# Performance work log

Hardware: AMD Instinct MI355X
Metric: run time of the kernel (lower is better)

The kernel has to match this reference:

```python
import jax, jax.numpy as jnp
import numpy as np

NUM_HEADS = 16

def alibi_slopes(num_heads):
    # 1 / ((2**8)**(1/H))**(i+1) for i in range(H)  -> shape (H, 1, 1)
    x = (2.0 ** 8) ** (1.0 / num_heads)
    return (1.0 / x ** (jnp.arange(1, num_heads + 1, dtype=jnp.float32)))[:, None, None]

def setup_inputs() -> dict:
    key = jax.random.key(0)
    k1, k2, k3 = jax.random.split(key, 3)
    B, T, D = 4, 2048, 1024
    x = jax.random.normal(k1, (B, T, D), dtype=jnp.float32)
    w_qkv = jax.random.normal(k2, (D, 3 * D), dtype=jnp.float32) * 0.02
    w_o = jax.random.normal(k3, (D, D), dtype=jnp.float32) * 0.02
    return {"x": x, "w_qkv": w_qkv, "w_o": w_o}

def reference(x, w_qkv, w_o):
    B, T, C = x.shape
    H = NUM_HEADS
    dh = C // H
    qkv = x @ w_qkv                                   # [B, T, 3C]
    q, k, v = jnp.split(qkv, 3, axis=-1)
    # b t (h d) -> b h t d
    q = q.reshape(B, T, H, dh).transpose(0, 2, 1, 3)
    k = k.reshape(B, T, H, dh).transpose(0, 2, 1, 3)
    v = v.reshape(B, T, H, dh).transpose(0, 2, 1, 3)
    wei = jnp.einsum('bhqd,bhkd->bhqk', q, k)         # [B, H, T, T]
    rel = (jnp.arange(T)[None, :] - jnp.arange(T)[:, None]).astype(jnp.float32)
    bias = alibi_slopes(H) * rel                      # [H, T, T]
    scale = jnp.float32(C) ** 0.5                     # note: full dim C, as in source
    scores = wei / scale + bias
    causal = jnp.tril(jnp.ones((T, T), dtype=bool))
    scores = jnp.where(causal, scores, jnp.float32(-jnp.inf))
    attn = jax.nn.softmax(scores, axis=-1)
    out = jnp.einsum('bhqk,bhkd->bhqd', attn, v)      # [B, H, T, dh]
    concat = out.transpose(0, 2, 1, 3).reshape(B, T, C)
    return concat @ w_o
```

## Files before the change

### kernel.cpp

```cpp
#include <hip/hip_runtime.h>
#include <hip/hip_bf16.h>

typedef float f32x4 __attribute__((ext_vector_type(4)));
typedef short bf16x8 __attribute__((ext_vector_type(8)));
typedef short bf16x4 __attribute__((ext_vector_type(4)));

static __device__ __forceinline__ short f2bs(float f) {
  __hip_bfloat16 h = __float2bfloat16(f);
  union { __hip_bfloat16 h; short s; } u;
  u.h = h;
  return u.s;
}

#define GLDS(gp, lp) __builtin_amdgcn_global_load_lds( \
    (const __attribute__((address_space(1))) unsigned int*)(gp), \
    (__attribute__((address_space(3))) unsigned int*)(lp), 16, 0, 0)

__global__ __launch_bounds__(256) void cvt_f32_bf16(const float* __restrict__ in,
                                                    short* __restrict__ out, int n4) {
  int i = blockIdx.x * 256 + threadIdx.x;
  if (i >= n4) return;
  f32x4 v = ((const f32x4*)in)[i];
  bf16x4 o;
  o[0] = f2bs(v[0]); o[1] = f2bs(v[1]); o[2] = f2bs(v[2]); o[3] = f2bs(v[3]);
  ((bf16x4*)out)[i] = o;
}

__global__ __launch_bounds__(256) void transpose_cvt(const float* __restrict__ in,
                                                     short* __restrict__ out,
                                                     int R, int C) {
  __shared__ float tile[32][33];
  int bx = blockIdx.x * 32;
  int by = blockIdx.y * 32;
  int tx = threadIdx.x & 31;
  int ty = threadIdx.x >> 5;
#pragma unroll
  for (int i = 0; i < 32; i += 8)
    tile[ty + i][tx] = in[(long)(by + ty + i) * C + bx + tx];
  __syncthreads();
#pragma unroll
  for (int i = 0; i < 32; i += 8)
    out[(long)(bx + ty + i) * R + by + tx] = f2bs(tile[tx][ty + i]);
}

__device__ __forceinline__ void gemm_mainloop(const short* __restrict__ A,
                                              const short* __restrict__ Bt,
                                              int K, int rowA0, int rowB0,
                                              short* As, short* Bs,
                                              f32x4 acc[4][4]) {
  const int tid = threadIdx.x;
  const int wave = tid >> 6;
  const int lane = tid & 63;
  const int lr = lane & 15;
  const int quad = lane >> 4;
  const short* aP = A + (long)(rowA0 + wave * 32 + (lane >> 2)) * K + (lane & 3) * 8;
  const short* bP = Bt + (long)(rowB0 + wave * 32 + (lane >> 2)) * K + (lane & 3) * 8;
  short* aL = As + wave * 32 * 32;
  short* bL = Bs + wave * 32 * 32;
  const int r0 = (wave >> 1) * 64;
  const int c0 = (wave & 1) * 64;
  const int c16K = 16 * K;
  for (int k0 = 0; k0 < K; k0 += 32) {
    GLDS(aP, aL);
    GLDS(aP + c16K, aL + 16 * 32);
    GLDS(bP, bL);
    GLDS(bP + c16K, bL + 16 * 32);
    __syncthreads();
    bf16x8 af[4], bfr[4];
#pragma unroll
    for (int i = 0; i < 4; ++i)
      af[i] = *(const bf16x8*)(As + (r0 + i * 16 + lr) * 32 + quad * 8);
#pragma unroll
    for (int j = 0; j < 4; ++j)
      bfr[j] = *(const bf16x8*)(Bs + (c0 + j * 16 + lr) * 32 + quad * 8);
#pragma unroll
    for (int i = 0; i < 4; ++i)
#pragma unroll
      for (int j = 0; j < 4; ++j)
        acc[i][j] = __builtin_amdgcn_mfma_f32_16x16x32_bf16(af[i], bfr[j], acc[i][j], 0, 0, 0);
    __syncthreads();
    aP += 32;
    bP += 32;
  }
}

__global__ __launch_bounds__(256) void gemm_qkv(const short* __restrict__ xb,
                                                const short* __restrict__ wT,
                                                short* __restrict__ q,
                                                short* __restrict__ k,
                                                short* __restrict__ vt) {
  __shared__ __align__(16) short As[128 * 32];
  __shared__ __align__(16) short Bs[128 * 32];
  f32x4 acc[4][4];
#pragma unroll
  for (int i = 0; i < 4; ++i)
#pragma unroll
    for (int j = 0; j < 4; ++j)
      acc[i][j] = (f32x4){0.f, 0.f, 0.f, 0.f};
  const int tileM = blockIdx.x * 128;
  const int tileN = blockIdx.y * 128;
  gemm_mainloop(xb, wT, 1024, tileM, tileN, As, Bs, acc);
  const int tid = threadIdx.x;
  const int wave = tid >> 6;
  const int lane = tid & 63;
  const int lr = lane & 15;
  const int quad = lane >> 4;
#pragma unroll
  for (int i = 0; i < 4; ++i) {
#pragma unroll
    for (int j = 0; j < 4; ++j) {
      int col = tileN + (wave & 1) * 64 + j * 16 + lr;
      int region = col >> 10;
      int w = col & 1023;
      int h = w >> 6;
      int d = w & 63;
#pragma unroll
      for (int r = 0; r < 4; ++r) {
        int row = tileM + (wave >> 1) * 64 + i * 16 + quad * 4 + r;
        int b = row >> 11;
        int t = row & 2047;
        long bh = b * 16 + h;
        float val = acc[i][j][r];
        if (region == 0)
          q[(bh * 2048 + t) * 64 + d] = f2bs(val * 0.03125f);
        else if (region == 1)
          k[(bh * 2048 + t) * 64 + d] = f2bs(val);
        else
          vt[(bh * 64 + d) * 2048 + t] = f2bs(val);
      }
    }
  }
}

__global__ __launch_bounds__(256, 5) void attn(const short* __restrict__ q,
                                               const short* __restrict__ kk,
                                               const short* __restrict__ vt,
                                               short* __restrict__ cat) {
  __shared__ __align__(16) short Ks[64 * 72];
  __shared__ __align__(16) short Vs[64 * 72];
  __shared__ __align__(16) short Ps[4 * 16 * 72];
  const int bx = blockIdx.x;
  const int j = 31 - (bx >> 6);
  const int bh = bx & 63;
  const int h = bh & 15;
  const int b = bh >> 4;
  const int tid = threadIdx.x;
  const int wave = tid >> 6;
  const int lane = tid & 63;
  const int lr = lane & 15;
  const int quad = lane >> 4;
  const float l2e = 1.44269504f;
  const float slope = exp2f(-0.5f * (float)(h + 1));
  const float slope_l2e = slope * l2e;
  const float c2 = -2.0f * l2e;
  const int d_cut = (int)ceilf(20.0f * exp2f(0.5f * (float)(h + 1)));
  const short* kbg = kk + (long)bh * 2048 * 64;
  const short* vbg = vt + (long)bh * 64 * 2048;
  const int srow = tid >> 3;
  const int scol = (tid & 7) * 8;
  short* pw = Ps + wave * 16 * 72;

  const int q0 = j * 64;
  const int mrow0 = q0 + wave * 16;
  const int kt_start = max(0, (q0 - d_cut) >> 6);
  const short* qptr = q + ((long)bh * 2048 + mrow0) * 64;
  bf16x8 qf0 = *(const bf16x8*)(qptr + (long)lr * 64 + quad * 8);
  bf16x8 qf1 = *(const bf16x8*)(qptr + (long)lr * 64 + 32 + quad * 8);
  float lp = 0.f;
  f32x4 O[4];
#pragma unroll
  for (int dt = 0; dt < 4; ++dt) O[dt] = (f32x4){0.f, 0.f, 0.f, 0.f};

  const short* kg = kbg + (long)kt_start * 64 * 64;
  const short* vg = vbg + kt_start * 64;
  bf16x8 pk0 = *(const bf16x8*)(kg + srow * 64 + scol);
  bf16x8 pk1 = *(const bf16x8*)(kg + (srow + 32) * 64 + scol);
  bf16x8 pv0 = *(const bf16x8*)(vg + (long)srow * 2048 + scol);
  bf16x8 pv1 = *(const bf16x8*)(vg + (long)(srow + 32) * 2048 + scol);
  for (int kt = kt_start; kt <= j; ++kt) {
    *(bf16x8*)(Ks + srow * 72 + scol) = pk0;
    *(bf16x8*)(Ks + (srow + 32) * 72 + scol) = pk1;
    *(bf16x8*)(Vs + srow * 72 + scol) = pv0;
    *(bf16x8*)(Vs + (srow + 32) * 72 + scol) = pv1;
    __syncthreads();
    if (kt < j) {
      const short* kg2 = kbg + (long)(kt + 1) * 64 * 64;
      const short* vg2 = vbg + (kt + 1) * 64;
      pk0 = *(const bf16x8*)(kg2 + srow * 64 + scol);
      pk1 = *(const bf16x8*)(kg2 + (srow + 32) * 64 + scol);
      pv0 = *(const bf16x8*)(vg2 + (long)srow * 2048 + scol);
      pv1 = *(const bf16x8*)(vg2 + (long)(srow + 32) * 2048 + scol);
    }
    const int kbase = kt * 64;
    f32x4 S[4];
#pragma unroll
    for (int ct = 0; ct < 4; ++ct) {
      bf16x8 kf0 = *(const bf16x8*)(Ks + (ct * 16 + lr) * 72 + quad * 8);
      bf16x8 kf1 = *(const bf16x8*)(Ks + (ct * 16 + lr) * 72 + 32 + quad * 8);
      f32x4 a = (f32x4){0.f, 0.f, 0.f, 0.f};
      a = __builtin_amdgcn_mfma_f32_16x16x32_bf16(kf0, qf0, a, 0, 0, 0);
      a = __builtin_amdgcn_mfma_f32_16x16x32_bf16(kf1, qf1, a, 0, 0, 0);
      S[ct] = a;
    }
    const bool diag = (kt == j);
    const float dbase = (float)(kbase - mrow0 - lr + quad * 4);
#pragma unroll
    for (int ct = 0; ct < 4; ++ct) {
      bf16x4 pkt;
#pragma unroll
      for (int r = 0; r < 4; ++r) {
        float dist = dbase + (float)(ct * 16 + r);
        float arg = fmaf(S[ct][r], l2e, fmaf(slope_l2e, dist, c2));
        if (diag) arg = (dist <= 0.f) ? arg : -10000.0f;
        float p = exp2f(arg);
        lp += p;
        pkt[r] = f2bs(p);
      }
      *(bf16x4*)(pw + lr * 72 + ct * 16 + quad * 4) = pkt;
    }
    asm volatile("s_waitcnt lgkmcnt(0)" ::: "memory");
    bf16x8 pf0 = *(const bf16x8*)(pw + lr * 72 + quad * 8);
    bf16x8 pf1 = *(const bf16x8*)(pw + lr * 72 + 32 + quad * 8);
#pragma unroll
    for (int dt = 0; dt < 4; ++dt) {
      bf16x8 vf0 = *(const bf16x8*)(Vs + (dt * 16 + lr) * 72 + quad * 8);
      bf16x8 vf1 = *(const bf16x8*)(Vs + (dt * 16 + lr) * 72 + 32 + quad * 8);
      O[dt] = __builtin_amdgcn_mfma_f32_16x16x32_bf16(pf0, vf0, O[dt], 0, 0, 0);
      O[dt] = __builtin_amdgcn_mfma_f32_16x16x32_bf16(pf1, vf1, O[dt], 0, 0, 0);
    }
    __syncthreads();
  }
  lp += __shfl_xor(lp, 16);
  lp += __shfl_xor(lp, 32);
#pragma unroll
  for (int r = 0; r < 4; ++r) {
    float lm = __shfl(lp, quad * 4 + r);
    float inv = 1.0f / lm;
    int t = mrow0 + quad * 4 + r;
#pragma unroll
    for (int dt = 0; dt < 4; ++dt)
      cat[((long)b * 2048 + t) * 1024 + h * 64 + dt * 16 + lr] =
          f2bs(O[dt][r] * inv);
  }
}

__global__ __launch_bounds__(256) void gemm_out(const short* __restrict__ cat,
                                                const short* __restrict__ woT,
                                                float* __restrict__ out) {
  __shared__ __align__(16) short As[128 * 32];
  __shared__ __align__(16) short Bs[128 * 32];
  f32x4 acc[4][4];
#pragma unroll
  for (int i = 0; i < 4; ++i)
#pragma unroll
    for (int j = 0; j < 4; ++j)
      acc[i][j] = (f32x4){0.f, 0.f, 0.f, 0.f};
  const int tileM = blockIdx.x * 128;
  const int tileN = blockIdx.y * 128;
  gemm_mainloop(cat, woT, 1024, tileM, tileN, As, Bs, acc);
  const int tid = threadIdx.x;
  const int wave = tid >> 6;
  const int lane = tid & 63;
  const int lr = lane & 15;
  const int quad = lane >> 4;
#pragma unroll
  for (int i = 0; i < 4; ++i)
#pragma unroll
    for (int j = 0; j < 4; ++j) {
      int col = tileN + (wave & 1) * 64 + j * 16 + lr;
#pragma unroll
      for (int r = 0; r < 4; ++r) {
        int row = tileM + (wave >> 1) * 64 + i * 16 + quad * 4 + r;
        out[(long)row * 1024 + col] = acc[i][j][r];
      }
    }
}

extern "C" void kernel_launch(void* const* d_in, const int* in_sizes, int n_in,
                              void* d_out, int out_size, void* d_ws, size_t ws_size,
                              hipStream_t stream) {
  const float* x = (const float*)d_in[0];
  const float* w_qkv = (const float*)d_in[1];
  const float* w_o = (const float*)d_in[2];
  float* out = (float*)d_out;
  short* ws = (short*)d_ws;
  short* xb = ws;
  short* wqkvT = xb + 8388608;
  short* woT = wqkvT + 3145728;
  short* q = woT + 1048576;
  short* kb = q + 8388608;
  short* vt = kb + 8388608;

  cvt_f32_bf16<<<8192, 256, 0, stream>>>(x, xb, 2097152);
  transpose_cvt<<<dim3(96, 32), 256, 0, stream>>>(w_qkv, wqkvT, 1024, 3072);
  transpose_cvt<<<dim3(32, 32), 256, 0, stream>>>(w_o, woT, 1024, 1024);
  gemm_qkv<<<dim3(64, 24), 256, 0, stream>>>(xb, wqkvT, q, kb, vt);
  attn<<<dim3(2048), 256, 0, stream>>>(q, kb, vt, xb );
  gemm_out<<<dim3(64, 8), 256, 0, stream>>>(xb, woT, out);
}
```

Baseline: 266.1 us.

## Double-buffer GEMM LDS tiles and vectorize V-transpose epilogue stores

The shared GEMM mainloop now uses two LDS buffers, so the global-to-LDS load for the next K step is issued before computing on the current one. This overlaps memory latency with MFMA work and drops one barrier per step. Both GEMM kernels get doubled shared arrays and a launch-bounds occupancy hint. The QKV epilogue hoists the row math and packs four consecutive t values into one 8-byte store for the transposed V. Doubling LDS use and the occupancy hint could limit resident blocks or cause register spilling.

```diff
diff --git a/kernel.cpp b/kernel.cpp
--- a/kernel.cpp
+++ b/kernel.cpp
@@ -41,6 +41,23 @@
 #pragma unroll
   for (int i = 0; i < 32; i += 8)
     out[(long)(bx + ty + i) * R + by + tx] = f2bs(tile[tx][ty + i]);
+}
+
+__device__ __forceinline__ void gemm_compute_tile(const short* Ac, const short* Bc,
+                                                  int r0, int c0, int lr, int quad,
+                                                  f32x4 acc[4][4]) {
+  bf16x8 af[4], bfr[4];
+#pragma unroll
+  for (int i = 0; i < 4; ++i)
+    af[i] = *(const bf16x8*)(Ac + (r0 + i * 16 + lr) * 32 + quad * 8);
+#pragma unroll
+  for (int j = 0; j < 4; ++j)
+    bfr[j] = *(const bf16x8*)(Bc + (c0 + j * 16 + lr) * 32 + quad * 8);
+#pragma unroll
+  for (int i = 0; i < 4; ++i)
+#pragma unroll
+    for (int j = 0; j < 4; ++j)
+      acc[i][j] = __builtin_amdgcn_mfma_f32_16x16x32_bf16(af[i], bfr[j], acc[i][j], 0, 0, 0);
 }
 
 __device__ __forceinline__ void gemm_mainloop(const short* __restrict__ A,
@@ -55,42 +72,47 @@
   const int quad = lane >> 4;
   const short* aP = A + (long)(rowA0 + wave * 32 + (lane >> 2)) * K + (lane & 3) * 8;
   const short* bP = Bt + (long)(rowB0 + wave * 32 + (lane >> 2)) * K + (lane & 3) * 8;
-  short* aL = As + wave * 32 * 32;
-  short* bL = Bs + wave * 32 * 32;
+  const int woff = wave * 32 * 32;
   const int r0 = (wave >> 1) * 64;
   const int c0 = (wave & 1) * 64;
   const int c16K = 16 * K;
-  for (int k0 = 0; k0 < K; k0 += 32) {
-    GLDS(aP, aL);
-    GLDS(aP + c16K, aL + 16 * 32);
-    GLDS(bP, bL);
-    GLDS(bP + c16K, bL + 16 * 32);
+  const int BUF = 128 * 32;
+  GLDS(aP, As + woff);
+  GLDS(aP + c16K, As + woff + 16 * 32);
+  GLDS(bP, Bs + woff);
+  GLDS(bP + c16K, Bs + woff + 16 * 32);
+  aP += 32; bP += 32;
+  const int nIter = K >> 5;
+#pragma unroll 1
+  for (int i = 0; i < nIter; i += 2) {
     __syncthreads();
-    bf16x8 af[4], bfr[4];
-#pragma unroll
-    for (int i = 0; i < 4; ++i)
-      af[i] = *(const bf16x8*)(As + (r0 + i * 16 + lr) * 32 + quad * 8);
-#pragma unroll
-    for (int j = 0; j < 4; ++j)
-      bfr[j] = *(const bf16x8*)(Bs + (c0 + j * 16 + lr) * 32 + quad * 8);
-#pragma unroll
-    for (int i = 0; i < 4; ++i)
-#pragma unroll
-      for (int j = 0; j < 4; ++j)
-        acc[i][j] = __builtin_amdgcn_mfma_f32_16x16x32_bf16(af[i], bfr[j], acc[i][j], 0, 0, 0);
+    if (i + 1 < nIter) {
+      GLDS(aP, As + BUF + woff);
+      GLDS(aP + c16K, As + BUF + woff + 16 * 32);
+      GLDS(bP, Bs + BUF + woff);
+      GLDS(bP + c16K, Bs + BUF + woff + 16 * 32);
+      aP += 32; bP += 32;
+    }
+    gemm_compute_tile(As, Bs, r0, c0, lr, quad, acc);
     __syncthreads();
-    aP += 32;
-    bP += 32;
+    if (i + 2 < nIter) {
+      GLDS(aP, As + woff);
+      GLDS(aP + c16K, As + woff + 16 * 32);
+      GLDS(bP, Bs + woff);
+      GLDS(bP + c16K, Bs + woff + 16 * 32);
+      aP += 32; bP += 32;
+    }
+    gemm_compute_tile(As + BUF, Bs + BUF, r0, c0, lr, quad, acc);
   }
 }
 
-__global__ __launch_bounds__(256) void gemm_qkv(const short* __restrict__ xb,
-                                                const short* __restrict__ wT,
-                                                short* __restrict__ q,
-                                                short* __restrict__ k,
-                                                short* __restrict__ vt) {
-  __shared__ __align__(16) short As[128 * 32];
-  __shared__ __align__(16) short Bs[128 * 32];
+__global__ __launch_bounds__(256, 5) void gemm_qkv(const short* __restrict__ xb,
+                                                   const short* __restrict__ wT,
+                                                   short* __restrict__ q,
+                                                   short* __restrict__ k,
+                                                   short* __restrict__ vt) {
+  __shared__ __align__(16) short As[2 * 128 * 32];
+  __shared__ __align__(16) short Bs[2 * 128 * 32];
   f32x4 acc[4][4];
 #pragma unroll
   for (int i = 0; i < 4; ++i)
@@ -107,6 +129,9 @@
   const int quad = lane >> 4;
 #pragma unroll
   for (int i = 0; i < 4; ++i) {
+    const int row0 = tileM + (wave >> 1) * 64 + i * 16 + quad * 4;
+    const int b = row0 >> 11;
+    const int t = row0 & 2047;
 #pragma unroll
     for (int j = 0; j < 4; ++j) {
       int col = tileN + (wave & 1) * 64 + j * 16 + lr;
@@ -114,19 +139,20 @@
       int w = col & 1023;
       int h = w >> 6;
       int d = w & 63;
-#pragma unroll
-      for (int r = 0; r < 4; ++r) {
-        int row = tileM + (wave >> 1) * 64 + i * 16 + quad * 4 + r;
-        int b = row >> 11;
-        int t = row & 2047;
-        long bh = b * 16 + h;
-        float val = acc[i][j][r];
-        if (region == 0)
-          q[(bh * 2048 + t) * 64 + d] = f2bs(val * 0.03125f);
-        else if (region == 1)
-          k[(bh * 2048 + t) * 64 + d] = f2bs(val);
-        else
-          vt[(bh * 64 + d) * 2048 + t] = f2bs(val);
+      long bh = (long)b * 16 + h;
+      if (region == 0) {
+#pragma unroll
+        for (int r = 0; r < 4; ++r)
+          q[(bh * 2048 + t + r) * 64 + d] = f2bs(acc[i][j][r] * 0.03125f);
+      } else if (region == 1) {
+#pragma unroll
+        for (int r = 0; r < 4; ++r)
+          k[(bh * 2048 + t + r) * 64 + d] = f2bs(acc[i][j][r]);
+      } else {
+        bf16x4 pk;
+#pragma unroll
+        for (int r = 0; r < 4; ++r) pk[r] = f2bs(acc[i][j][r]);
+        *(bf16x4*)(vt + (bh * 64 + d) * 2048 + t) = pk;
       }
     }
   }
@@ -244,11 +270,11 @@
   }
 }
 
-__global__ __launch_bounds__(256) void gemm_out(const short* __restrict__ cat,
-                                                const short* __restrict__ woT,
-                                                float* __restrict__ out) {
-  __shared__ __align__(16) short As[128 * 32];
-  __shared__ __align__(16) short Bs[128 * 32];
+__global__ __launch_bounds__(256, 5) void gemm_out(const short* __restrict__ cat,
+                                                   const short* __restrict__ woT,
+                                                   float* __restrict__ out) {
+  __shared__ __align__(16) short As[2 * 128 * 32];
+  __shared__ __align__(16) short Bs[2 * 128 * 32];
   f32x4 acc[4][4];
 #pragma unroll
   for (int i = 0; i < 4; ++i)
```

Result: no change. 265.4 us (-0.3%).
